# Kernel optimization log

Hardware: AMD Instinct MI355X
Metric: run time of the kernel (lower is better)

## Reference

```python
import jax, jax.numpy as jnp
import numpy as np

NUM_EDGE_CLASS = 4
NODE_DIM = 64
BATCH = 32
NUM_NODES = 1024


def setup_inputs() -> dict:
    key = jax.random.key(0)
    k1, k2, k3, k4, k5 = jax.random.split(key, 5)
    node_state = jax.random.normal(k1, (BATCH, NUM_NODES, NODE_DIM), dtype=jnp.float32)
    adj_mat = jax.random.randint(k2, (BATCH, NUM_NODES, NUM_NODES), 0, NUM_EDGE_CLASS, dtype=jnp.int32)
    matrix_in = jax.random.normal(k3, (NUM_EDGE_CLASS, NODE_DIM, NODE_DIM), dtype=jnp.float32) * 0.1
    matrix_out = jax.random.normal(k4, (NUM_EDGE_CLASS, NODE_DIM, NODE_DIM), dtype=jnp.float32) * 0.1
    bias = jax.random.normal(k5, (2 * NODE_DIM,), dtype=jnp.float32)
    return {"node_state": node_state, "adj_mat": adj_mat,
            "matrix_in": matrix_in, "matrix_out": matrix_out, "bias": bias}


def reference(node_state, adj_mat, matrix_in, matrix_out, bias):
    """GGNN message passing (Li et al. Eq. 2).

    Original TF code builds a [b, n*d, n*d] block matrix where block (i, j)
    is matrix_in[adj_mat[b, i, j]] (and matrix_out[adj_mat[b, j, i]] for the
    outgoing direction), then matmuls against flattened node states. The
    equivalent fused math is:
      m_in[b,i]  = sum_j matrix_in[adj[b,i,j]]  @ h[b,j]
      m_out[b,i] = sum_j matrix_out[adj[b,j,i]] @ h[b,j]
    Implemented via a one-hot over the (small) set of edge classes so the
    per-edge d x d matrices are never materialized per edge.
    """
    h = node_state  # [b, n, d]
    onehot = jax.nn.one_hot(adj_mat, NUM_EDGE_CLASS, dtype=h.dtype)  # [b, n, n, c]
    # per-class neighbor aggregation, then one small matmul per class
    s_in = jnp.einsum('bijc,bje->bice', onehot, h)          # [b, n, c, d]
    m_in = jnp.einsum('bice,cde->bid', s_in, matrix_in)      # [b, n, d]
    s_out = jnp.einsum('bjic,bje->bice', onehot, h)          # transposed adjacency
    m_out = jnp.einsum('bice,cde->bid', s_out, matrix_out)   # [b, n, d]
    message = jnp.concatenate([m_in, m_out], axis=-1) + bias  # [b, n, 2d]
    return message
```

## Files before the change

kernel.cpp:

```cpp
#include <hip/hip_runtime.h>


namespace {

typedef unsigned int  u32;
typedef unsigned short u16;
typedef __attribute__((ext_vector_type(8))) short bf16x8;
typedef __attribute__((ext_vector_type(4))) float f32x4;

constexpr int NN = 1024;
constexpr int ND = 64;

__device__ inline u16 f2bf(float x) {
    u32 u = __float_as_uint(x);
    return (u16)((u + 0x7FFFu + ((u >> 16) & 1u)) >> 16);
}
__device__ inline float bf2f(u16 x) { return __uint_as_float(((u32)x) << 16); }

#if defined(__has_builtin)
#if __has_builtin(__builtin_amdgcn_global_load_lds)
#define HAVE_GLL 1
#endif
#endif

__device__ inline void async_copy16(const void* g, void* l) {
#ifdef HAVE_GLL
    typedef __attribute__((address_space(1))) const u32 gu32;
    typedef __attribute__((address_space(3))) u32 lu32;
    __builtin_amdgcn_global_load_lds((gu32*)g, (lu32*)l, 16, 0, 0);
#else
    int lane = threadIdx.x & 63;
    ((uint4*)l)[lane] = *(const uint4*)((const char*)g);
#endif
}

__global__ __launch_bounds__(256) void pack_adj(
    const int* __restrict__ adj, u32* __restrict__ adjP, u32* __restrict__ adjPT)
{
    __shared__ u32 rp[64][16];
    const int t = threadIdx.x;
    const int bid = blockIdx.x;
    const int b = bid >> 6, It = (bid >> 4) & 3, Jt = (bid >> 2) & 3, s = bid & 3;
    const int* base = adj + ((size_t)b << 20) + (size_t)(It * 256 + s * 64) * NN + Jt * 256;

    const int row = t >> 2, seg = t & 3;
    const int* rptr = base + (size_t)row * NN + seg * 64;
    u32 w[4];
    #pragma unroll
    for (int q = 0; q < 4; ++q) {
        int4 v0 = *(const int4*)(rptr + q * 16 + 0);
        int4 v1 = *(const int4*)(rptr + q * 16 + 4);
        int4 v2 = *(const int4*)(rptr + q * 16 + 8);
        int4 v3 = *(const int4*)(rptr + q * 16 + 12);
        u32 u = (u32)(v0.x & 3) | ((u32)(v0.y & 3) << 2) | ((u32)(v0.z & 3) << 4) | ((u32)(v0.w & 3) << 6)
              | ((u32)(v1.x & 3) << 8) | ((u32)(v1.y & 3) << 10) | ((u32)(v1.z & 3) << 12) | ((u32)(v1.w & 3) << 14)
              | ((u32)(v2.x & 3) << 16) | ((u32)(v2.y & 3) << 18) | ((u32)(v2.z & 3) << 20) | ((u32)(v2.w & 3) << 22)
              | ((u32)(v3.x & 3) << 24) | ((u32)(v3.y & 3) << 26) | ((u32)(v3.z & 3) << 28) | ((u32)(v3.w & 3) << 30);
        w[q] = u;
    }
    u32* op = adjP + (((((size_t)b * 4 + Jt) * 16 + It * 4 + s) * 4 + seg) * 64 + row) * 4;
    *(uint4*)op = make_uint4(w[0], w[1], w[2], w[3]);
    *(uint4*)&rp[row][seg * 4] = make_uint4(w[0], w[1], w[2], w[3]);
    __syncthreads();

    const int sc = t >> 6, il = t & 63;
    const int cw = sc * 4 + (il >> 4);
    const int bp = (il & 15) * 2;
    u32 o[4];
    #pragma unroll
    for (int jj = 0; jj < 4; ++jj) {
        u32 acc = 0;
        #pragma unroll
        for (int k = 0; k < 16; ++k)
            acc |= ((rp[jj * 16 + k][cw] >> bp) & 3u) << (2 * k);
        o[jj] = acc;
    }
    u32* op2 = adjPT + (((((size_t)b * 4 + It) * 16 + Jt * 4 + sc) * 4 + s) * 64 + il) * 4;
    *(uint4*)op2 = make_uint4(o[0], o[1], o[2], o[3]);
}

__global__ __launch_bounds__(256) void prep_h(
    const float* __restrict__ h, u16* __restrict__ Hws, float* __restrict__ PA)
{
    __shared__ u16 hl[256][72];
    const int t = threadIdx.x;
    const int b = blockIdx.x >> 2, jc = blockIdx.x & 3;
    const float* hb = h + ((size_t)b * NN + jc * 256) * ND;
    #pragma unroll
    for (int k = 0; k < 16; ++k) {
        int j = k * 16 + (t >> 4);
        int e4 = (t & 15) * 4;
        float4 v = *(const float4*)(hb + (size_t)j * ND + e4);
        *(u32*)&hl[j][e4]     = (u32)f2bf(v.x) | ((u32)f2bf(v.y) << 16);
        *(u32*)&hl[j][e4 + 2] = (u32)f2bf(v.z) | ((u32)f2bf(v.w) << 16);
    }
    __syncthreads();
    u16* ob = Hws + (size_t)(b * 4 + jc) * 2048 * 8;
    const int e = t & 63;
    float psum = 0.f;
    #pragma unroll
    for (int k = 0; k < 8; ++k) {
        int u = k * 4 + (t >> 6);
        u32 p0, p1, p2, p3;
        u16 x0 = hl[u * 8 + 0][e], x1 = hl[u * 8 + 1][e], x2 = hl[u * 8 + 2][e], x3 = hl[u * 8 + 3][e];
        u16 x4 = hl[u * 8 + 4][e], x5 = hl[u * 8 + 5][e], x6 = hl[u * 8 + 6][e], x7 = hl[u * 8 + 7][e];
        psum += bf2f(x0) + bf2f(x1) + bf2f(x2) + bf2f(x3) + bf2f(x4) + bf2f(x5) + bf2f(x6) + bf2f(x7);
        p0 = (u32)x0 | ((u32)x1 << 16); p1 = (u32)x2 | ((u32)x3 << 16);
        p2 = (u32)x4 | ((u32)x5 << 16); p3 = (u32)x6 | ((u32)x7 << 16);
        *(uint4*)(ob + (size_t)(u * 64 + e) * 8) = make_uint4(p0, p1, p2, p3);
    }
    atomicAdd(&PA[b * 64 + e], psum);
}

__global__ __launch_bounds__(256) void prep_m(
    const float* __restrict__ Min, const float* __restrict__ Mout,
    const float* __restrict__ bias, const float* __restrict__ PA,
    u16* __restrict__ Mws, float* __restrict__ basews)
{
    const int t = threadIdx.x, bb = blockIdx.x;
    if (bb == 0) {
        for (int i = t; i < 2 * 4096; i += 256) {
            const float* M = (i < 4096) ? Min : Mout;
            int idx = i & 4095;
            float m0 = M[idx], m1 = M[4096 + idx], m2 = M[8192 + idx], m3 = M[12288 + idx];
            u16* o = Mws + (size_t)(i >> 12) * 3 * 4096;
            o[idx]            = f2bf(m1 - m0);
            o[4096 + idx]     = f2bf(m2 - m0);
            o[8192 + idx]     = f2bf(m0 - m1 - m2 + m3);
        }
    }
    if (t < 128) {
        int d = t & 63, dir = t >> 6;
        const float* M0 = (dir ? Mout : Min) + d * 64;
        float s = bias[dir * 64 + d];
        #pragma unroll 8
        for (int e = 0; e < 64; ++e) s += PA[bb * 64 + e] * M0[e];
        basews[(bb * 2 + dir) * 64 + d] = s;
    }
}

__global__ __launch_bounds__(256, 4) void ggnn_main(
    const u32* __restrict__ adjP, const u32* __restrict__ adjPT,
    const u16* __restrict__ Hws, const u16* __restrict__ Mws,
    const float* __restrict__ basews, float* __restrict__ out)
{
    __shared__ __align__(16) char smem[36864];
    char* adjL = smem;
    char* hL   = smem + 4096;
    u16 (*Sb)[16][72] = (u16(*)[16][72])smem;

    const int t = threadIdx.x;
    const int w = t >> 6, lane = t & 63;
    const int ln = t & 15, qd = (t & 63) >> 4, qd2 = qd >> 1;
    const int shamt = (qd & 1) * 16;
    const int bid = blockIdx.x;
    const int dir = bid >> 9;
    const int b = (bid >> 4) & 31, it = bid & 15;

    const u32* Adir = dir ? adjPT : adjP;
    f32x4 acc[3][4];
    #pragma unroll
    for (int p = 0; p < 3; ++p)
        #pragma unroll
        for (int nt = 0; nt < 4; ++nt) acc[p][nt] = (f32x4){0.f, 0.f, 0.f, 0.f};

    for (int jc = 0; jc < 4; ++jc) {
        __syncthreads();
        const char* at = (const char*)(Adir + (size_t)((b * 4 + jc) * 16 + it) * 1024);
        const char* ht = (const char*)(Hws + (size_t)(b * 4 + jc) * 16384);
        if (w == 0) {
            #pragma unroll
            for (int u = 0; u < 4; ++u)
                async_copy16(at + u * 1024 + lane * 16, adjL + u * 1024);
        }
        #pragma unroll
        for (int k = 0; k < 8; ++k) {
            int i = w + k * 4;
            async_copy16(ht + i * 1024 + lane * 16, hL + i * 1024);
        }
        __syncthreads();

        uint4 Ar[4];
        #pragma unroll
        for (int u = 0; u < 4; ++u)
            Ar[u] = *(const uint4*)(adjL + (u * 64 + w * 16 + ln) * 16);

        #pragma unroll
        for (int ks = 0; ks < 8; ++ks) {
            uint4 Q = Ar[ks >> 1];
            u32 a = (ks & 1) ? (qd2 ? Q.w : Q.z) : (qd2 ? Q.y : Q.x);
            u32 f  = (a >> shamt) & 0xFFFFu;
            u32 x0 = f & 0x5555u;
            u32 x1 = (f >> 1) & 0x5555u;
            u32 xt = x0 & x1;
            bf16x8 bf[4];
            #pragma unroll
            for (int nt = 0; nt < 4; ++nt)
                bf[nt] = *(const bf16x8*)(hL + ((ks * 4 + qd) * 64 + nt * 16 + ln) * 16);
            #pragma unroll
            for (int p = 0; p < 3; ++p) {
                u32 xp = (p == 0) ? x0 : (p == 1) ? x1 : xt;
                union { u32 u[4]; bf16x8 v; } A;
                #pragma unroll
                for (int wd = 0; wd < 4; ++wd) {
                    u32 z = xp >> (4 * wd);
                    A.u[wd] = ((z & 1u) | ((z & 4u) << 14)) * 0x3F80u;
                }
                #pragma unroll
                for (int nt = 0; nt < 4; ++nt)
                    acc[p][nt] = __builtin_amdgcn_mfma_f32_16x16x32_bf16(
                        A.v, bf[nt], acc[p][nt], 0, 0, 0);
            }
        }
    }

    __syncthreads();

    #pragma unroll
    for (int p = 0; p < 3; ++p)
        #pragma unroll
        for (int nt = 0; nt < 4; ++nt)
            #pragma unroll
            for (int r = 0; r < 4; ++r)
                Sb[w * 3 + p][qd * 4 + r][nt * 16 + ln] = f2bf(acc[p][nt][r]);

    const float* bv = basews + (b * 2 + dir) * 64;
    f32x4 acc2[4];
    #pragma unroll
    for (int dt = 0; dt < 4; ++dt) {
        float v = bv[dt * 16 + ln];
        acc2[dt] = (f32x4){v, v, v, v};
    }
    const u16* Mb = Mws + (size_t)dir * 3 * 4096;
    #pragma unroll
    for (int p = 0; p < 3; ++p) {
        #pragma unroll
        for (int ks2 = 0; ks2 < 2; ++ks2) {
            bf16x8 af = *(const bf16x8*)&Sb[w * 3 + p][ln][ks2 * 32 + qd * 8];
            #pragma unroll
            for (int dt = 0; dt < 4; ++dt) {
                bf16x8 mf = *(const bf16x8*)(Mb + (size_t)(p * 64 + dt * 16 + ln) * 64
                                             + ks2 * 32 + qd * 8);
                acc2[dt] = __builtin_amdgcn_mfma_f32_16x16x32_bf16(af, mf, acc2[dt], 0, 0, 0);
            }
        }
    }
    #pragma unroll
    for (int dt = 0; dt < 4; ++dt)
        #pragma unroll
        for (int r = 0; r < 4; ++r)
            out[((size_t)b * NN + it * 64 + w * 16 + qd * 4 + r) * 128
                + dir * 64 + dt * 16 + ln] = acc2[dt][r];
}

}

extern "C" void kernel_launch(void* const* d_in, const int* in_sizes, int n_in,
                              void* d_out, int out_size, void* d_ws, size_t ws_size,
                              hipStream_t stream) {
    (void)in_sizes; (void)n_in; (void)out_size; (void)ws_size;
    const float* h    = (const float*)d_in[0];
    const int*   adj  = (const int*)d_in[1];
    const float* Min  = (const float*)d_in[2];
    const float* Mout = (const float*)d_in[3];
    const float* bias = (const float*)d_in[4];
    float* out = (float*)d_out;

    char* ws = (char*)d_ws;
    u32* adjP   = (u32*)(ws + 0);
    u32* adjPT  = (u32*)(ws + 8388608);
    u16* Hws    = (u16*)(ws + 16777216);
    float* PA   = (float*)(ws + 20971520);
    u16* Mws    = (u16*)(ws + 20979712);
    float* basews = (float*)(ws + 21028864);

    hipMemsetAsync(PA, 0, 32 * 64 * sizeof(float), stream);
    pack_adj<<<2048, 256, 0, stream>>>(adj, adjP, adjPT);
    prep_h<<<128, 256, 0, stream>>>(h, Hws, PA);
    prep_m<<<32, 256, 0, stream>>>(Min, Mout, bias, PA, Mws, basews);
    ggnn_main<<<1024, 256, 0, stream>>>(adjP, adjPT, Hws, Mws, basews, out);
}
```

Baseline: 262.1 us.

## Load adjacency and H fragments directly from global instead of staging in LDS

Drops the async global-to-LDS staging of adjacency and packed H tiles in the main kernel. Each lane now reads its MFMA fragments straight from global memory (relying on cache), which removes two barriers per jc iteration and shrinks shared memory to the epilogue buffer. The occupancy hint in launch_bounds is removed and the MFMA issue order is interleaved across the three classes. The risk is redundant global and L2 traffic, since all four waves reread the same H tile, and higher exposed load latency without the staging.

```diff
diff --git a/kernel.cpp b/kernel.cpp
--- a/kernel.cpp
+++ b/kernel.cpp
@@ -17,21 +17,8 @@
 }
 __device__ inline float bf2f(u16 x) { return __uint_as_float(((u32)x) << 16); }
 
-#if defined(__has_builtin)
-#if __has_builtin(__builtin_amdgcn_global_load_lds)
-#define HAVE_GLL 1
-#endif
-#endif
-
-__device__ inline void async_copy16(const void* g, void* l) {
-#ifdef HAVE_GLL
-    typedef __attribute__((address_space(1))) const u32 gu32;
-    typedef __attribute__((address_space(3))) u32 lu32;
-    __builtin_amdgcn_global_load_lds((gu32*)g, (lu32*)l, 16, 0, 0);
-#else
-    int lane = threadIdx.x & 63;
-    ((uint4*)l)[lane] = *(const uint4*)((const char*)g);
-#endif
+__device__ inline u32 oh2(u32 z) {
+    return ((z & 1u) | ((z & 4u) << 14)) * 0x3F80u;
 }
 
 __global__ __launch_bounds__(256) void pack_adj(
@@ -101,12 +88,11 @@
     #pragma unroll
     for (int k = 0; k < 8; ++k) {
         int u = k * 4 + (t >> 6);
-        u32 p0, p1, p2, p3;
         u16 x0 = hl[u * 8 + 0][e], x1 = hl[u * 8 + 1][e], x2 = hl[u * 8 + 2][e], x3 = hl[u * 8 + 3][e];
         u16 x4 = hl[u * 8 + 4][e], x5 = hl[u * 8 + 5][e], x6 = hl[u * 8 + 6][e], x7 = hl[u * 8 + 7][e];
         psum += bf2f(x0) + bf2f(x1) + bf2f(x2) + bf2f(x3) + bf2f(x4) + bf2f(x5) + bf2f(x6) + bf2f(x7);
-        p0 = (u32)x0 | ((u32)x1 << 16); p1 = (u32)x2 | ((u32)x3 << 16);
-        p2 = (u32)x4 | ((u32)x5 << 16); p3 = (u32)x6 | ((u32)x7 << 16);
+        u32 p0 = (u32)x0 | ((u32)x1 << 16), p1 = (u32)x2 | ((u32)x3 << 16);
+        u32 p2 = (u32)x4 | ((u32)x5 << 16), p3 = (u32)x6 | ((u32)x7 << 16);
         *(uint4*)(ob + (size_t)(u * 64 + e) * 8) = make_uint4(p0, p1, p2, p3);
     }
     atomicAdd(&PA[b * 64 + e], psum);
@@ -124,9 +110,9 @@
             int idx = i & 4095;
             float m0 = M[idx], m1 = M[4096 + idx], m2 = M[8192 + idx], m3 = M[12288 + idx];
             u16* o = Mws + (size_t)(i >> 12) * 3 * 4096;
-            o[idx]            = f2bf(m1 - m0);
-            o[4096 + idx]     = f2bf(m2 - m0);
-            o[8192 + idx]     = f2bf(m0 - m1 - m2 + m3);
+            o[idx]        = f2bf(m1 - m0);
+            o[4096 + idx] = f2bf(m2 - m0);
+            o[8192 + idx] = f2bf(m0 - m1 - m2 + m3);
         }
     }
     if (t < 128) {
@@ -139,18 +125,15 @@
     }
 }
 
-__global__ __launch_bounds__(256, 4) void ggnn_main(
+__global__ __launch_bounds__(256) void ggnn_main(
     const u32* __restrict__ adjP, const u32* __restrict__ adjPT,
     const u16* __restrict__ Hws, const u16* __restrict__ Mws,
     const float* __restrict__ basews, float* __restrict__ out)
 {
-    __shared__ __align__(16) char smem[36864];
-    char* adjL = smem;
-    char* hL   = smem + 4096;
-    u16 (*Sb)[16][72] = (u16(*)[16][72])smem;
+    __shared__ u16 Sb[12][16][72];
 
     const int t = threadIdx.x;
-    const int w = t >> 6, lane = t & 63;
+    const int w = t >> 6;
     const int ln = t & 15, qd = (t & 63) >> 4, qd2 = qd >> 1;
     const int shamt = (qd & 1) * 16;
     const int bid = blockIdx.x;
@@ -165,56 +148,43 @@
         for (int nt = 0; nt < 4; ++nt) acc[p][nt] = (f32x4){0.f, 0.f, 0.f, 0.f};
 
     for (int jc = 0; jc < 4; ++jc) {
-        __syncthreads();
-        const char* at = (const char*)(Adir + (size_t)((b * 4 + jc) * 16 + it) * 1024);
-        const char* ht = (const char*)(Hws + (size_t)(b * 4 + jc) * 16384);
-        if (w == 0) {
-            #pragma unroll
-            for (int u = 0; u < 4; ++u)
-                async_copy16(at + u * 1024 + lane * 16, adjL + u * 1024);
-        }
-        #pragma unroll
-        for (int k = 0; k < 8; ++k) {
-            int i = w + k * 4;
-            async_copy16(ht + i * 1024 + lane * 16, hL + i * 1024);
-        }
-        __syncthreads();
+        const u32* at = Adir + (size_t)((b * 4 + jc) * 16 + it) * 1024;
+        const u16* ht = Hws + (size_t)(b * 4 + jc) * 16384;
 
         uint4 Ar[4];
         #pragma unroll
         for (int u = 0; u < 4; ++u)
-            Ar[u] = *(const uint4*)(adjL + (u * 64 + w * 16 + ln) * 16);
+            Ar[u] = *(const uint4*)(at + (u * 64 + w * 16 + ln) * 4);
 
         #pragma unroll
         for (int ks = 0; ks < 8; ++ks) {
+            bf16x8 bf[4];
+            #pragma unroll
+            for (int nt = 0; nt < 4; ++nt)
+                bf[nt] = *(const bf16x8*)(ht + (size_t)((ks * 4 + qd) * 64 + nt * 16 + ln) * 8);
+
             uint4 Q = Ar[ks >> 1];
             u32 a = (ks & 1) ? (qd2 ? Q.w : Q.z) : (qd2 ? Q.y : Q.x);
-            u32 f  = (a >> shamt) & 0xFFFFu;
+            u32 f = (a >> shamt) & 0xFFFFu;
             u32 x0 = f & 0x5555u;
             u32 x1 = (f >> 1) & 0x5555u;
             u32 xt = x0 & x1;
-            bf16x8 bf[4];
-            #pragma unroll
-            for (int nt = 0; nt < 4; ++nt)
-                bf[nt] = *(const bf16x8*)(hL + ((ks * 4 + qd) * 64 + nt * 16 + ln) * 16);
-            #pragma unroll
-            for (int p = 0; p < 3; ++p) {
-                u32 xp = (p == 0) ? x0 : (p == 1) ? x1 : xt;
-                union { u32 u[4]; bf16x8 v; } A;
-                #pragma unroll
-                for (int wd = 0; wd < 4; ++wd) {
-                    u32 z = xp >> (4 * wd);
-                    A.u[wd] = ((z & 1u) | ((z & 4u) << 14)) * 0x3F80u;
-                }
-                #pragma unroll
-                for (int nt = 0; nt < 4; ++nt)
-                    acc[p][nt] = __builtin_amdgcn_mfma_f32_16x16x32_bf16(
-                        A.v, bf[nt], acc[p][nt], 0, 0, 0);
+
+            union { u32 u[4]; bf16x8 v; } A0, A1, AT;
+            #pragma unroll
+            for (int wd = 0; wd < 4; ++wd) {
+                A0.u[wd] = oh2(x0 >> (4 * wd));
+                A1.u[wd] = oh2(x1 >> (4 * wd));
+                AT.u[wd] = oh2(xt >> (4 * wd));
+            }
+            #pragma unroll
+            for (int nt = 0; nt < 4; ++nt) {
+                acc[0][nt] = __builtin_amdgcn_mfma_f32_16x16x32_bf16(A0.v, bf[nt], acc[0][nt], 0, 0, 0);
+                acc[1][nt] = __builtin_amdgcn_mfma_f32_16x16x32_bf16(A1.v, bf[nt], acc[1][nt], 0, 0, 0);
+                acc[2][nt] = __builtin_amdgcn_mfma_f32_16x16x32_bf16(AT.v, bf[nt], acc[2][nt], 0, 0, 0);
             }
         }
     }
-
-    __syncthreads();
 
     #pragma unroll
     for (int p = 0; p < 3; ++p)
```

Result: slower. 270.4 us (+3.2%).
